# Kernel optimization log

Measured on AMD Instinct MI355X. Metric: run time of the kernel, lower is better.

The kernel has to match this reference:

```python
import jax, jax.numpy as jnp
import numpy as np

N, D, H = 4096, 1024, 8
DH = D // H
EPS = 1e-5


def layer_norm(x, g, b):
    mu = jnp.mean(x, axis=-1, keepdims=True)
    var = jnp.mean(jnp.square(x - mu), axis=-1, keepdims=True)
    return (x - mu) * jax.lax.rsqrt(var + EPS) * g + b


def setup_inputs() -> dict:
    key = jax.random.key(0)
    ks = jax.random.split(key, 12)
    s = 0.02
    inp = {
        "x": jax.random.normal(ks[0], (N, D), dtype=jnp.float32),
        "adj": (jax.random.uniform(ks[1], (N, N)) < 0.01).astype(jnp.float32),
        "Wq": jax.random.normal(ks[2], (D, D), dtype=jnp.float32) * s,
        "Wk": jax.random.normal(ks[3], (D, D), dtype=jnp.float32) * s,
        "Wv": jax.random.normal(ks[4], (D, D), dtype=jnp.float32) * s,
        "Wo_w": jax.random.normal(ks[5], (D, D), dtype=jnp.float32) * s,
        "Wo_b": jnp.zeros((D,), dtype=jnp.float32),
        "adj_bias": jnp.full((H,), 1.0, dtype=jnp.float32),
        "ln1_g": jnp.ones((D,), dtype=jnp.float32),
        "ln1_b": jnp.zeros((D,), dtype=jnp.float32),
        "ffn_ln_g": jnp.ones((D,), dtype=jnp.float32),
        "ffn_ln_b": jnp.zeros((D,), dtype=jnp.float32),
        "ffn_w1": jax.random.normal(ks[6], (D, 2 * D), dtype=jnp.float32) * s,
        "ffn_b1": jnp.zeros((2 * D,), dtype=jnp.float32),
        "ffn_w2": jax.random.normal(ks[7], (2 * D, D), dtype=jnp.float32) * s,
        "ffn_b2": jnp.zeros((D,), dtype=jnp.float32),
    }
    return inp


def reference(x, adj, Wq, Wk, Wv, Wo_w, Wo_b, adj_bias, ln1_g, ln1_b,
              ffn_ln_g, ffn_ln_b, ffn_w1, ffn_b1, ffn_w2, ffn_b2):
    scale = DH ** -0.5
    Q = (x @ Wq).reshape(N, H, DH)
    K = (x @ Wk).reshape(N, H, DH)
    V = (x @ Wv).reshape(N, H, DH)
    # attn[i,h,j] = <Q_i, K_j> * scale + beta_h * adj[i,j]
    attn = jnp.einsum('bhd,nhd->bhn', Q, K) * scale
    attn = attn + adj_bias[None, :, None] * adj[:, None, :]
    attn = jax.nn.softmax(attn, axis=-1)  # dropout in eval mode -> identity
    out = jnp.einsum('bhn,nhd->bhd', attn, V).reshape(N, D)
    out = out @ Wo_w + Wo_b
    h = layer_norm(x + out, ln1_g, ln1_b)
    f = layer_norm(h, ffn_ln_g, ffn_ln_b)
    f = jax.nn.gelu(f @ ffn_w1 + ffn_b1, approximate=False) @ ffn_w2 + ffn_b2
    return h + f
```

## Files before the change

### kernel.cpp

```cpp
#include <hip/hip_runtime.h>
#include <hip/hip_bf16.h>
#include <cstdint>
#include <cstddef>

typedef __hip_bfloat16 bf16;
typedef __attribute__((ext_vector_type(8))) short short8;
typedef __attribute__((ext_vector_type(4))) short short4v;
typedef __attribute__((ext_vector_type(4))) float floatx4;
typedef unsigned long long u64;

#define DEVI static __device__ __forceinline__

DEVI void load_lds16(const void* g, void* l) {
  __builtin_amdgcn_global_load_lds((const __attribute__((address_space(1))) unsigned int*)g,
                                   (__attribute__((address_space(3))) unsigned int*)l, 16, 0, 0);
}
DEVI short8 ld8(const bf16* p) { return *(const short8*)p; }
DEVI floatx4 mfma16(short8 a, short8 b, floatx4 c) {
  return __builtin_amdgcn_mfma_f32_16x16x32_bf16(a, b, c, 0, 0, 0);
}
DEVI floatx4 mfma1k(short4v a, short4v b, floatx4 c) {
  return __builtin_amdgcn_mfma_f32_16x16x16bf16_1k(a, b, c, 0, 0, 0);
}
DEVI short bfb(float f) { bf16 h = __float2bfloat16(f); return __builtin_bit_cast(short, h); }
DEVI float fbf(short s) { bf16 h = __builtin_bit_cast(bf16, s); return __bfloat162float(h); }

DEVI void tr_tile(const float* in, bf16* out, int R, int C, int bx, int by) {
  __shared__ float t[32][33];
  int c0 = bx * 32, r0 = by * 32;
  int tx = threadIdx.x & 31, ty = threadIdx.x >> 5;
#pragma unroll
  for (int i = 0; i < 32; i += 8) t[ty + i][tx] = in[(size_t)(r0 + ty + i) * C + c0 + tx];
  __syncthreads();
#pragma unroll
  for (int i = 0; i < 32; i += 8)
    out[(size_t)(c0 + ty + i) * R + r0 + tx] = __float2bfloat16(t[tx][ty + i]);
}

__global__ __launch_bounds__(256)
void prep_all(const float* __restrict__ x, bf16* __restrict__ xb,
              const float* __restrict__ adj, u64* __restrict__ bits,
              const float* Wq, const float* Wk, const float* Wv, const float* Wo,
              const float* W1, const float* W2,
              bf16* Wqkvt, bf16* Wot, bf16* W1t, bf16* W2t) {
  int id = blockIdx.x;
  if (id < 4096) {
    const int row = id, tid = threadIdx.x;
    const int wave = tid >> 6, lane = tid & 63;
    float4 v = ((const float4*)(x + (size_t)row * 1024))[tid];
    bf16* o = xb + (size_t)row * 1024 + tid * 4;
    o[0] = __float2bfloat16(v.x); o[1] = __float2bfloat16(v.y);
    o[2] = __float2bfloat16(v.z); o[3] = __float2bfloat16(v.w);
    const float* arow = adj + (size_t)row * 4096;
#pragma unroll
    for (int it = 0; it < 16; it++) {
      int col = it * 256 + tid;
      u64 m = __ballot(arow[col] != 0.f);
      if (lane == 0) bits[(size_t)row * 64 + it * 4 + wave] = m;
    }
  } else if (id < 8192) {
    int q = id - 4096, w = q >> 10, t = q & 1023;
    const float* in = w == 0 ? Wq : w == 1 ? Wk : w == 2 ? Wv : Wo;
    bf16* out = w == 0 ? Wqkvt : w == 1 ? Wqkvt + 1024ull * 1024
              : w == 2 ? Wqkvt + 2048ull * 1024 : Wot;
    tr_tile(in, out, 1024, 1024, t & 31, t >> 5);
  } else if (id < 10240) {
    int t = id - 8192;
    tr_tile(W1, W1t, 1024, 2048, t & 63, t >> 6);
  } else {
    int t = id - 10240;
    tr_tile(W2, W2t, 2048, 1024, t & 31, t >> 5);
  }
}

__global__ __launch_bounds__(256)
void tr_bf16t(const bf16* __restrict__ in, bf16* __restrict__ out, int inLd) {
  __shared__ bf16 t[32][33];
  int c0 = blockIdx.x * 32, r0 = blockIdx.y * 32;
  int tx = threadIdx.x, ty = threadIdx.y;
#pragma unroll
  for (int i = 0; i < 32; i += 8) t[ty + i][tx] = in[(size_t)(r0 + ty + i) * inLd + c0 + tx];
  __syncthreads();
#pragma unroll
  for (int i = 0; i < 32; i += 8)
    out[(size_t)(c0 + ty + i) * 4096 + r0 + tx] = t[tx][ty + i];
}

template <int MODE, int BN>
__global__ __launch_bounds__(256)
void gemm_bt(const bf16* __restrict__ A, const bf16* __restrict__ Bt,
             const float* __restrict__ bias, const float* __restrict__ resid,
             float* __restrict__ outF, bf16* __restrict__ outB,
             int M, int Nn, int K) {
  constexpr int NI = BN / 32;
  __shared__ alignas(16) bf16 As[3][128 * 32];
  __shared__ alignas(16) bf16 Bs[3][BN * 32];
  const int tid = threadIdx.x;
  const int wave = tid >> 6, lane = tid & 63;
  const int m0 = blockIdx.y * 128, n0 = blockIdx.x * BN;
  const int wr = (wave >> 1) * 64, wc = (wave & 1) * (BN / 2);
  const int l15 = lane & 15, qq = lane >> 4;
  const int lr = lane >> 2, l4 = lane & 3;
  const int T = K >> 5;

  floatx4 acc[4][NI];
#pragma unroll
  for (int i = 0; i < 4; i++)
#pragma unroll
    for (int j = 0; j < NI; j++) acc[i][j] = (floatx4)0.f;

  const bf16* gA0 = A + (size_t)(m0 + wave * 16 + lr) * K + l4 * 8;
  const bf16* gA1 = gA0 + (size_t)64 * K;
  const bf16* gB0 = Bt + (size_t)(n0 + wave * 16 + lr) * K + l4 * 8;
  const bf16* gB1 = gB0 + (size_t)64 * K;
  const int lo = wave * 16 * 32;

  auto stage = [&](int t, int buf) {
    int kt = t * 32;
    load_lds16(gA0 + kt, &As[buf][lo]);
    load_lds16(gA1 + kt, &As[buf][64 * 32 + lo]);
    load_lds16(gB0 + kt, &Bs[buf][lo]);
    if (BN == 128) load_lds16(gB1 + kt, &Bs[buf][64 * 32 + lo]);
  };
  stage(0, 0);
  stage(1, 1);

  int bc = 0;
  for (int t = 0; t < T; ++t) {
    if (t < T - 1) {
      if constexpr (BN == 128)
        asm volatile("s_waitcnt vmcnt(4) lgkmcnt(0)" ::: "memory");
      else
        asm volatile("s_waitcnt vmcnt(3) lgkmcnt(0)" ::: "memory");
    } else {
      asm volatile("s_waitcnt vmcnt(0) lgkmcnt(0)" ::: "memory");
    }
    __builtin_amdgcn_s_barrier();
    if (t + 2 < T) { int bs = bc == 0 ? 2 : bc - 1; stage(t + 2, bs); }

    short8 af[4], bfr[NI];
#pragma unroll
    for (int mi = 0; mi < 4; mi++) af[mi] = ld8(&As[bc][(wr + mi * 16 + l15) * 32 + qq * 8]);
#pragma unroll
    for (int ni = 0; ni < NI; ni++) bfr[ni] = ld8(&Bs[bc][(wc + ni * 16 + l15) * 32 + qq * 8]);
#pragma unroll
    for (int mi = 0; mi < 4; mi++)
#pragma unroll
      for (int ni = 0; ni < NI; ni++)
        acc[mi][ni] = mfma16(af[mi], bfr[ni], acc[mi][ni]);
    bc = bc == 2 ? 0 : bc + 1;
  }

#pragma unroll
  for (int mi = 0; mi < 4; mi++) {
    int row = m0 + wr + mi * 16 + qq * 4;
#pragma unroll
    for (int ni = 0; ni < NI; ni++) {
      int col = n0 + wc + ni * 16 + l15;
      float bv = (MODE >= 1) ? bias[col] : 0.f;
#pragma unroll
      for (int r = 0; r < 4; r++) {
        float v = acc[mi][ni][r] + bv;
        size_t off = (size_t)(row + r) * Nn + col;
        if (MODE == 0) {
          outB[off] = __float2bfloat16(v);
        } else if (MODE == 2) {
          outB[off] = __float2bfloat16(0.5f * v * (1.f + erff(v * 0.70710678118654752f)));
        } else if (MODE == 1) {
          outF[off] = v;
        } else {
          outF[off] = v + resid[off];
        }
      }
    }
  }
}

__global__ __launch_bounds__(256, 2)
void attn_kernel(const bf16* __restrict__ QKV, const bf16* __restrict__ Vt,
                 const u64* __restrict__ adjbits, const float* __restrict__ adj_bias,
                 bf16* __restrict__ AOpart, float* __restrict__ lpart) {
  __shared__ alignas(16) bf16 Kf[2][16 * 512];
  __shared__ alignas(16) bf16 Vf[2][16 * 512];
  const int q0 = blockIdx.x * 128;
  const int h = blockIdx.y;
  const int split = blockIdx.z;
  const int k0 = split * 1024;
  const int tid = threadIdx.x, wave = tid >> 6, lane = tid & 63;
  const int l15 = lane & 15, qq = lane >> 4;
  const float log2e = 1.4426950408889634f;
  const float beta2 = adj_bias[h] * log2e;
  const float scale2 = 0.08838834764831845f * log2e;

  short8 qf[2][4];
#pragma unroll
  for (int mi = 0; mi < 2; mi++)
#pragma unroll
    for (int kk = 0; kk < 4; kk++)
      qf[mi][kk] = ld8(&QKV[(size_t)(q0 + wave * 32 + mi * 16 + l15) * 3072 +
                            h * 128 + kk * 32 + qq * 8]);

  floatx4 o[2][8];
#pragma unroll
  for (int mi = 0; mi < 2; mi++)
#pragma unroll
    for (int d = 0; d < 8; d++) o[mi][d] = (floatx4)0.f;
  float lrow[2] = {0.f, 0.f};

  const size_t abase = (size_t)(q0 + wave * 32 + l15) * 64 + split * 16;

  auto stage = [&](int t, int buf) {
    const int kt = k0 + t * 64;
#pragma unroll
    for (int i = 0; i < 4; i++) {
      int fi = wave * 4 + i;
      int ni = fi >> 2, kk = fi & 3;
      load_lds16(&QKV[(size_t)(kt + ni * 16 + l15) * 3072 + 1024 + h * 128 + kk * 32 + qq * 8],
                 (char*)Kf[buf] + fi * 1024);
      int d = fi >> 1, k2 = fi & 1;
      load_lds16(&Vt[(size_t)(h * 128 + d * 16 + l15) * 4096 + kt + k2 * 32 + qq * 8],
                 (char*)Vf[buf] + fi * 1024);
    }
  };

  stage(0, 0);
  u64 a0c = adjbits[abase];
  u64 a1c = adjbits[abase + 1024];

  for (int t = 0; t < 16; t++) {
    __syncthreads();
    if (t < 15) stage(t + 1, (t + 1) & 1);
    u64 a0n = 0, a1n = 0;
    if (t < 15) { a0n = adjbits[abase + t + 1]; a1n = adjbits[abase + 1024 + t + 1]; }

    const bf16* Kc = Kf[t & 1];
    const bf16* Vc = Vf[t & 1];
    const uint32_t w0lo = (uint32_t)a0c, w0hi = (uint32_t)(a0c >> 32);
    const uint32_t w1lo = (uint32_t)a1c, w1hi = (uint32_t)(a1c >> 32);

#pragma unroll
    for (int ni = 0; ni < 4; ni++) {
      floatx4 s0 = (floatx4)0.f, s1 = (floatx4)0.f;
#pragma unroll
      for (int kk = 0; kk < 4; kk++) {
        short8 kfr = ld8(&Kc[(ni * 4 + kk) * 512 + lane * 8]);
        s0 = mfma16(kfr, qf[0][kk], s0);
        s1 = mfma16(kfr, qf[1][kk], s1);
      }
      short4v pa0, pa1;
      {
        const uint32_t u0 = (ni >= 2 ? w0hi : w0lo) >> ((ni & 1) * 16);
        const uint32_t u1 = (ni >= 2 ? w1hi : w1lo) >> ((ni & 1) * 16);
        const int bp = qq * 4;
        float p0, p1, p2, p3;
        p0 = __builtin_amdgcn_exp2f(fmaf(s0[0], scale2, ((u0 >> (bp + 0)) & 1) ? beta2 : 0.f));
        p1 = __builtin_amdgcn_exp2f(fmaf(s0[1], scale2, ((u0 >> (bp + 1)) & 1) ? beta2 : 0.f));
        p2 = __builtin_amdgcn_exp2f(fmaf(s0[2], scale2, ((u0 >> (bp + 2)) & 1) ? beta2 : 0.f));
        p3 = __builtin_amdgcn_exp2f(fmaf(s0[3], scale2, ((u0 >> (bp + 3)) & 1) ? beta2 : 0.f));
        lrow[0] += (p0 + p1) + (p2 + p3);
        pa0.x = bfb(p0); pa0.y = bfb(p1); pa0.z = bfb(p2); pa0.w = bfb(p3);
        p0 = __builtin_amdgcn_exp2f(fmaf(s1[0], scale2, ((u1 >> (bp + 0)) & 1) ? beta2 : 0.f));
        p1 = __builtin_amdgcn_exp2f(fmaf(s1[1], scale2, ((u1 >> (bp + 1)) & 1) ? beta2 : 0.f));
        p2 = __builtin_amdgcn_exp2f(fmaf(s1[2], scale2, ((u1 >> (bp + 2)) & 1) ? beta2 : 0.f));
        p3 = __builtin_amdgcn_exp2f(fmaf(s1[3], scale2, ((u1 >> (bp + 3)) & 1) ? beta2 : 0.f));
        lrow[1] += (p0 + p1) + (p2 + p3);
        pa1.x = bfb(p0); pa1.y = bfb(p1); pa1.z = bfb(p2); pa1.w = bfb(p3);
      }
      const int voff = ((ni & 1) * 2 + (qq >> 1)) * 256 + l15 * 16 + (qq & 1) * 8;
#pragma unroll
      for (int d = 0; d < 8; d++) {
        short4v vf = *(const short4v*)((const char*)Vc + (d * 2 + (ni >> 1)) * 1024 + voff);
        o[0][d] = mfma1k(pa0, vf, o[0][d]);
        o[1][d] = mfma1k(pa1, vf, o[1][d]);
      }
    }
    a0c = a0n; a1c = a1n;
  }

#pragma unroll
  for (int mi = 0; mi < 2; mi++) {
    float v = lrow[mi];
    v += __shfl_xor(v, 16, 64);
    v += __shfl_xor(v, 32, 64);
    if (qq == 0) lpart[((size_t)split * 4096 + q0 + wave * 32 + mi * 16 + l15) * 8 + h] = v;
#pragma unroll
    for (int r = 0; r < 4; r++) {
      int grow = q0 + wave * 32 + mi * 16 + qq * 4 + r;
      bf16* dst = AOpart + ((size_t)split * 4096 + grow) * 1024 + h * 128;
#pragma unroll
      for (int d = 0; d < 8; d++) dst[d * 16 + l15] = __float2bfloat16(o[mi][d][r]);
    }
  }
}

__global__ __launch_bounds__(256)
void attn_norm(const bf16* __restrict__ AOpart, const float* __restrict__ lpart,
               bf16* __restrict__ AO) {
  int row = blockIdx.x, tid = threadIdx.x;
  int h = tid >> 5;
  float ls = 0.f;
#pragma unroll
  for (int s = 0; s < 4; s++) ls += lpart[((size_t)s * 4096 + row) * 8 + h];
  float a0 = 0.f, a1 = 0.f, a2 = 0.f, a3 = 0.f;
#pragma unroll
  for (int s = 0; s < 4; s++) {
    short4v v = *(const short4v*)&AOpart[((size_t)s * 4096 + row) * 1024 + tid * 4];
    a0 += fbf(v.x); a1 += fbf(v.y); a2 += fbf(v.z); a3 += fbf(v.w);
  }
  float inv = 1.f / ls;
  bf16* op = AO + (size_t)row * 1024 + tid * 4;
  op[0] = __float2bfloat16(a0 * inv);
  op[1] = __float2bfloat16(a1 * inv);
  op[2] = __float2bfloat16(a2 * inv);
  op[3] = __float2bfloat16(a3 * inv);
}

DEVI void block_sum2(float& a, float& b, float* red) {
#pragma unroll
  for (int o = 1; o < 64; o <<= 1) { a += __shfl_xor(a, o, 64); b += __shfl_xor(b, o, 64); }
  int wv = threadIdx.x >> 6;
  if ((threadIdx.x & 63) == 0) { red[wv] = a; red[4 + wv] = b; }
  __syncthreads();
  a = red[0] + red[1] + red[2] + red[3];
  b = red[4] + red[5] + red[6] + red[7];
  __syncthreads();
}

__global__ __launch_bounds__(256)
void ln2_kernel(const float* __restrict__ x, const float* __restrict__ ao,
                const float* __restrict__ g1, const float* __restrict__ b1,
                const float* __restrict__ g2, const float* __restrict__ b2,
                float* __restrict__ hout, bf16* __restrict__ fln) {
  __shared__ float red[8];
  const int row = blockIdx.x, tid = threadIdx.x;
  float4 xv = ((const float4*)(x + (size_t)row * 1024))[tid];
  float4 av = ((const float4*)(ao + (size_t)row * 1024))[tid];
  float s0 = xv.x + av.x, s1 = xv.y + av.y, s2 = xv.z + av.z, s3 = xv.w + av.w;
  float sum = s0 + s1 + s2 + s3;
  float ssq = s0 * s0 + s1 * s1 + s2 * s2 + s3 * s3;
  block_sum2(sum, ssq, red);
  float mu = sum * (1.f / 1024.f);
  float rs = rsqrtf(ssq * (1.f / 1024.f) - mu * mu + 1e-5f);
  float4 gv = ((const float4*)g1)[tid], bv = ((const float4*)b1)[tid];
  float h0 = (s0 - mu) * rs * gv.x + bv.x;
  float h1 = (s1 - mu) * rs * gv.y + bv.y;
  float h2 = (s2 - mu) * rs * gv.z + bv.z;
  float h3 = (s3 - mu) * rs * gv.w + bv.w;
  float4 hv; hv.x = h0; hv.y = h1; hv.z = h2; hv.w = h3;
  ((float4*)(hout + (size_t)row * 1024))[tid] = hv;
  float sum2 = h0 + h1 + h2 + h3;
  float ssq2 = h0 * h0 + h1 * h1 + h2 * h2 + h3 * h3;
  block_sum2(sum2, ssq2, red);
  float mu2 = sum2 * (1.f / 1024.f);
  float rs2 = rsqrtf(ssq2 * (1.f / 1024.f) - mu2 * mu2 + 1e-5f);
  float4 g2v = ((const float4*)g2)[tid], b2v = ((const float4*)b2)[tid];
  bf16* op = fln + (size_t)row * 1024 + tid * 4;
  op[0] = __float2bfloat16((h0 - mu2) * rs2 * g2v.x + b2v.x);
  op[1] = __float2bfloat16((h1 - mu2) * rs2 * g2v.y + b2v.y);
  op[2] = __float2bfloat16((h2 - mu2) * rs2 * g2v.z + b2v.z);
  op[3] = __float2bfloat16((h3 - mu2) * rs2 * g2v.w + b2v.w);
}

extern "C" void kernel_launch(void* const* d_in, const int* in_sizes, int n_in,
                              void* d_out, int out_size, void* d_ws, size_t ws_size,
                              hipStream_t stream) {
  const float* x    = (const float*)d_in[0];
  const float* adj  = (const float*)d_in[1];
  const float* Wq   = (const float*)d_in[2];
  const float* Wk   = (const float*)d_in[3];
  const float* Wv   = (const float*)d_in[4];
  const float* Wo   = (const float*)d_in[5];
  const float* Wob  = (const float*)d_in[6];
  const float* adjb = (const float*)d_in[7];
  const float* g1   = (const float*)d_in[8];
  const float* b1   = (const float*)d_in[9];
  const float* g2   = (const float*)d_in[10];
  const float* b2   = (const float*)d_in[11];
  const float* W1   = (const float*)d_in[12];
  const float* fb1  = (const float*)d_in[13];
  const float* W2   = (const float*)d_in[14];
  const float* fb2  = (const float*)d_in[15];
  float* out = (float*)d_out;

  char* w = (char*)d_ws;
  size_t off = 0;
  auto take = [&](size_t bytes) {
    char* p = w + off;
    off += (bytes + 255) & ~(size_t)255;
    return p;
  };
  bf16* xb    = (bf16*)take(4096ull * 1024 * 2);
  bf16* Wqkvt = (bf16*)take(3072ull * 1024 * 2);
  bf16* Wot   = (bf16*)take(1024ull * 1024 * 2);
  bf16* W1t   = (bf16*)take(2048ull * 1024 * 2);
  bf16* W2t   = (bf16*)take(1024ull * 2048 * 2);
  bf16* QKV   = (bf16*)take(4096ull * 3072 * 2);
  bf16* Vt    = (bf16*)take(1024ull * 4096 * 2);
  bf16* AO    = (bf16*)take(4096ull * 1024 * 2);
  u64*  adjbits = (u64*)take(4096ull * 64 * 8);
  float* lpart  = (float*)take(4ull * 4096 * 8 * 4);
  char* big = take(32ull << 20);
  bf16*  AOpart = (bf16*)big;
  float* WoP    = (float*)big;
  float* H   = (float*)take(4096ull * 1024 * 4);
  bf16*  FLN = (bf16*)take(4096ull * 1024 * 2);
  bf16*  G   = (bf16*)take(4096ull * 2048 * 2);

  dim3 tb(32, 8);
  prep_all<<<12288, 256, 0, stream>>>(x, xb, adj, adjbits, Wq, Wk, Wv, Wo, W1, W2,
                                      Wqkvt, Wot, W1t, W2t);
  gemm_bt<0, 128><<<dim3(24, 32), 256, 0, stream>>>(xb, Wqkvt, nullptr, nullptr,
                                                    nullptr, QKV, 4096, 3072, 1024);
  tr_bf16t<<<dim3(32, 128), tb, 0, stream>>>(QKV + 2048, Vt, 3072);
  attn_kernel<<<dim3(32, 8, 4), 256, 0, stream>>>(QKV, Vt, adjbits, adjb, AOpart, lpart);
  attn_norm<<<4096, 256, 0, stream>>>(AOpart, lpart, AO);
  gemm_bt<1, 64><<<dim3(16, 32), 256, 0, stream>>>(AO, Wot, Wob, nullptr,
                                                   WoP, nullptr, 4096, 1024, 1024);
  ln2_kernel<<<4096, 256, 0, stream>>>(x, WoP, g1, b1, g2, b2, H, FLN);
  gemm_bt<2, 128><<<dim3(16, 32), 256, 0, stream>>>(FLN, W1t, fb1, nullptr,
                                                    nullptr, G, 4096, 2048, 1024);
  gemm_bt<3, 64><<<dim3(16, 32), 256, 0, stream>>>(G, W2t, fb2, H,
                                                   out, nullptr, 4096, 1024, 2048);
}
```

Baseline: 431.0 us.

## Split attention work across 8 waves with one 16-row query tile each

The attention kernel now launches 512 threads per block, and each wave handles 16 query rows instead of 32. This halves the per-wave accumulators, Q fragments and adjacency words, and the K/V staging is spread over twice as many waves. The goal is lower register pressure and more resident waves to hide MFMA, exp and LDS latency. In exchange, each K/V fragment read from LDS is reused by only one query tile instead of two, which doubles LDS read traffic per unit of compute.

Measured after the change: 433.0 us. No clear change (+0.5%).

```diff
diff --git a/kernel.cpp b/kernel.cpp
--- a/kernel.cpp
+++ b/kernel.cpp
@@ -176,7 +176,7 @@
   }
 }
 
-__global__ __launch_bounds__(256, 2)
+__global__ __launch_bounds__(512, 4)
 void attn_kernel(const bf16* __restrict__ QKV, const bf16* __restrict__ Vt,
                  const u64* __restrict__ adjbits, const float* __restrict__ adj_bias,
                  bf16* __restrict__ AOpart, float* __restrict__ lpart) {
@@ -192,28 +192,23 @@
   const float beta2 = adj_bias[h] * log2e;
   const float scale2 = 0.08838834764831845f * log2e;
 
-  short8 qf[2][4];
-#pragma unroll
-  for (int mi = 0; mi < 2; mi++)
-#pragma unroll
-    for (int kk = 0; kk < 4; kk++)
-      qf[mi][kk] = ld8(&QKV[(size_t)(q0 + wave * 32 + mi * 16 + l15) * 3072 +
-                            h * 128 + kk * 32 + qq * 8]);
-
-  floatx4 o[2][8];
-#pragma unroll
-  for (int mi = 0; mi < 2; mi++)
-#pragma unroll
-    for (int d = 0; d < 8; d++) o[mi][d] = (floatx4)0.f;
-  float lrow[2] = {0.f, 0.f};
-
-  const size_t abase = (size_t)(q0 + wave * 32 + l15) * 64 + split * 16;
+  short8 qf[4];
+#pragma unroll
+  for (int kk = 0; kk < 4; kk++)
+    qf[kk] = ld8(&QKV[(size_t)(q0 + wave * 16 + l15) * 3072 + h * 128 + kk * 32 + qq * 8]);
+
+  floatx4 o[8];
+#pragma unroll
+  for (int d = 0; d < 8; d++) o[d] = (floatx4)0.f;
+  float lrow = 0.f;
+
+  const size_t abase = (size_t)(q0 + wave * 16 + l15) * 64 + split * 16;
 
   auto stage = [&](int t, int buf) {
     const int kt = k0 + t * 64;
 #pragma unroll
-    for (int i = 0; i < 4; i++) {
-      int fi = wave * 4 + i;
+    for (int i = 0; i < 2; i++) {
+      int fi = wave * 2 + i;
       int ni = fi >> 2, kk = fi & 3;
       load_lds16(&QKV[(size_t)(kt + ni * 16 + l15) * 3072 + 1024 + h * 128 + kk * 32 + qq * 8],
                  (char*)Kf[buf] + fi * 1024);
@@ -225,70 +220,58 @@
 
   stage(0, 0);
   u64 a0c = adjbits[abase];
-  u64 a1c = adjbits[abase + 1024];
 
   for (int t = 0; t < 16; t++) {
     __syncthreads();
     if (t < 15) stage(t + 1, (t + 1) & 1);
-    u64 a0n = 0, a1n = 0;
-    if (t < 15) { a0n = adjbits[abase + t + 1]; a1n = adjbits[abase + 1024 + t + 1]; }
+    u64 a0n = 0;
+    if (t < 15) a0n = adjbits[abase + t + 1];
 
     const bf16* Kc = Kf[t & 1];
     const bf16* Vc = Vf[t & 1];
     const uint32_t w0lo = (uint32_t)a0c, w0hi = (uint32_t)(a0c >> 32);
-    const uint32_t w1lo = (uint32_t)a1c, w1hi = (uint32_t)(a1c >> 32);
 
 #pragma unroll
     for (int ni = 0; ni < 4; ni++) {
-      floatx4 s0 = (floatx4)0.f, s1 = (floatx4)0.f;
+      floatx4 s0 = (floatx4)0.f;
 #pragma unroll
       for (int kk = 0; kk < 4; kk++) {
         short8 kfr = ld8(&Kc[(ni * 4 + kk) * 512 + lane * 8]);
-        s0 = mfma16(kfr, qf[0][kk], s0);
-        s1 = mfma16(kfr, qf[1][kk], s1);
+        s0 = mfma16(kfr, qf[kk], s0);
       }
-      short4v pa0, pa1;
+      short4v pa0;
       {
         const uint32_t u0 = (ni >= 2 ? w0hi : w0lo) >> ((ni & 1) * 16);
-        const uint32_t u1 = (ni >= 2 ? w1hi : w1lo) >> ((ni & 1) * 16);
         const int bp = qq * 4;
         float p0, p1, p2, p3;
         p0 = __builtin_amdgcn_exp2f(fmaf(s0[0], scale2, ((u0 >> (bp + 0)) & 1) ? beta2 : 0.f));
         p1 = __builtin_amdgcn_exp2f(fmaf(s0[1], scale2, ((u0 >> (bp + 1)) & 1) ? beta2 : 0.f));
         p2 = __builtin_amdgcn_exp2f(fmaf(s0[2], scale2, ((u0 >> (bp + 2)) & 1) ? beta2 : 0.f));
         p3 = __builtin_amdgcn_exp2f(fmaf(s0[3], scale2, ((u0 >> (bp + 3)) & 1) ? beta2 : 0.f));
-        lrow[0] += (p0 + p1) + (p2 + p3);
+        lrow += (p0 + p1) + (p2 + p3);
         pa0.x = bfb(p0); pa0.y = bfb(p1); pa0.z = bfb(p2); pa0.w = bfb(p3);
-        p0 = __builtin_amdgcn_exp2f(fmaf(s1[0], scale2, ((u1 >> (bp + 0)) & 1) ? beta2 : 0.f));
-        p1 = __builtin_amdgcn_exp2f(fmaf(s1[1], scale2, ((u1 >> (bp + 1)) & 1) ? beta2 : 0.f));
-        p2 = __builtin_amdgcn_exp2f(fmaf(s1[2], scale2, ((u1 >> (bp + 2)) & 1) ? beta2 : 0.f));
-        p3 = __builtin_amdgcn_exp2f(fmaf(s1[3], scale2, ((u1 >> (bp + 3)) & 1) ? beta2 : 0.f));
-        lrow[1] += (p0 + p1) + (p2 + p3);
-        pa1.x = bfb(p0); pa1.y = bfb(p1); pa1.z = bfb(p2); pa1.w = bfb(p3);
       }
       const int voff = ((ni & 1) * 2 + (qq >> 1)) * 256 + l15 * 16 + (qq & 1) * 8;
 #pragma unroll
       for (int d = 0; d < 8; d++) {
         short4v vf = *(const short4v*)((const char*)Vc + (d * 2 + (ni >> 1)) * 1024 + voff);
-        o[0][d] = mfma1k(pa0, vf, o[0][d]);
-        o[1][d] = mfma1k(pa1, vf, o[1][d]);
+        o[d] = mfma1k(pa0, vf, o[d]);
       }
     }
-    a0c = a0n; a1c = a1n;
-  }
-
-#pragma unroll
-  for (int mi = 0; mi < 2; mi++) {
-    float v = lrow[mi];
+    a0c = a0n;
+  }
+
+  {
+    float v = lrow;
     v += __shfl_xor(v, 16, 64);
     v += __shfl_xor(v, 32, 64);
-    if (qq == 0) lpart[((size_t)split * 4096 + q0 + wave * 32 + mi * 16 + l15) * 8 + h] = v;
+    if (qq == 0) lpart[((size_t)split * 4096 + q0 + wave * 16 + l15) * 8 + h] = v;
 #pragma unroll
     for (int r = 0; r < 4; r++) {
-      int grow = q0 + wave * 32 + mi * 16 + qq * 4 + r;
+      int grow = q0 + wave * 16 + qq * 4 + r;
       bf16* dst = AOpart + ((size_t)split * 4096 + grow) * 1024 + h * 128;
 #pragma unroll
-      for (int d = 0; d < 8; d++) dst[d * 16 + l15] = __float2bfloat16(o[mi][d][r]);
+      for (int d = 0; d < 8; d++) dst[d * 16 + l15] = __float2bfloat16(o[d][r]);
     }
   }
 }
@@ -412,7 +395,7 @@
   gemm_bt<0, 128><<<dim3(24, 32), 256, 0, stream>>>(xb, Wqkvt, nullptr, nullptr,
                                                     nullptr, QKV, 4096, 3072, 1024);
   tr_bf16t<<<dim3(32, 128), tb, 0, stream>>>(QKV + 2048, Vt, 3072);
-  attn_kernel<<<dim3(32, 8, 4), 256, 0, stream>>>(QKV, Vt, adjbits, adjb, AOpart, lpart);
+  attn_kernel<<<dim3(32, 8, 4), 512, 0, stream>>>(QKV, Vt, adjbits, adjb, AOpart, lpart);
   attn_norm<<<4096, 256, 0, stream>>>(AOpart, lpart, AO);
   gemm_bt<1, 64><<<dim3(16, 32), 256, 0, stream>>>(AO, Wot, Wob, nullptr,
                                                    WoP, nullptr, 4096, 1024, 1024);
```
